# Kernel tuning notes

Measured on AMD Instinct MI355X. Metric: run time of the kernel, lower is better.

Reference implementation:

```python
import jax, jax.numpy as jnp
import numpy as np

N_FFT = 1024
N_STAGES = 3
N_SUB = N_FFT >> N_STAGES      # 128-point base IDFT
N_CHUNKS = 1 << N_STAGES       # 8 chunks after partial bit-reversal


def _mod_seq(order):
    mset = [0]
    for o in range(order):
        step = 2 ** o
        mset = [v for x in mset for v in (x, x + step)]
    return mset


def _perm_matrix(N, order):
    m = np.zeros((N, N), dtype=np.float32)
    base = 2 ** order
    k = 0
    for p in _mod_seq(order):
        for j in range(N // base):
            m[j * base + p, k] = 1.0
            k += 1
    return m


PERM = jnp.asarray(_perm_matrix(N_FFT, N_STAGES))
_idft = np.fft.ifft(np.eye(N_SUB))
IDFT_R = jnp.asarray(_idft.real.astype(np.float32))
IDFT_I = jnp.asarray(_idft.imag.astype(np.float32))


def _twiddle(n_fft_stage):
    w = np.exp(2j * np.pi / n_fft_stage) ** np.arange(n_fft_stage // 2)  # inverse sign
    return (jnp.asarray(w.real.astype(np.float32)),
            jnp.asarray(w.imag.astype(np.float32)))


TWIDDLES = []
_stage_size = N_FFT // 2 ** (N_STAGES - 1)
for _ in range(N_STAGES):
    TWIDDLES.append(_twiddle(_stage_size))
    _stage_size *= 2


def _idft_apply(re, im):
    yr = re @ IDFT_R.T - im @ IDFT_I.T
    yi = re @ IDFT_I.T + im @ IDFT_R.T
    return yr, yi


def _ifft_forward(re, im):
    # partial bit-reversal permutation then chunk
    re_p = jnp.split(re @ PERM, N_CHUNKS, axis=-1)
    im_p = jnp.split(im @ PERM, N_CHUNKS, axis=-1)
    ev_r, ev_i, od_r, od_i = [], [], [], []
    for j in range(N_CHUNKS // 2):
        er, ei = _idft_apply(re_p[2 * j], im_p[2 * j])
        o_r, o_i = _idft_apply(re_p[2 * j + 1], im_p[2 * j + 1])
        ev_r.append(er); ev_i.append(ei); od_r.append(o_r); od_i.append(o_i)
    # butterfly twiddle stages
    for tr, ti in TWIDDLES:
        ner, nei, nor, noi = [], [], [], []
        for i in range(len(ev_r)):
            todd_r = tr * od_r[i] - ti * od_i[i]
            todd_i = tr * od_i[i] + ti * od_r[i]
            real = jnp.concatenate([ev_r[i] + todd_r, ev_r[i] - todd_r], axis=-1)
            imag = jnp.concatenate([ev_i[i] + todd_i, ev_i[i] - todd_i], axis=-1)
            if i % 2 == 0:
                ner.append(real); nei.append(imag)
            else:
                nor.append(real); noi.append(imag)
        ev_r, ev_i, od_r, od_i = ner, nei, nor, noi
    scale = 1.0 / (1 << N_STAGES)  # IFFTNormalizer
    return ev_r[0] * scale, ev_i[0] * scale


def setup_inputs() -> dict:
    key = jax.random.key(0)
    k1, k2 = jax.random.split(key)
    re = jax.random.normal(k1, (8, 4096, N_FFT), dtype=jnp.float32)
    im = jax.random.normal(k2, (8, 4096, N_FFT), dtype=jnp.float32)
    return {"re": re, "im": im}


def reference(re, im):
    return _ifft_forward(re, im)
```

## Files before the change

### kernel.cpp

```cpp
#include <hip/hip_runtime.h>

#define NFFT 1024
#define NT   256
__device__ __forceinline__ int swz(int a) { return a + (a >> 5); }

template<int L, int M>
__device__ __forceinline__ void stage(const float* __restrict__ xr,
                                      const float* __restrict__ xi,
                                      float* __restrict__ yr,
                                      float* __restrict__ yi,
                                      int t) {
    const int k  = t & (M - 1);
    const int j  = t / M;
    const int rb = swz(t);

    float c0r = xr[rb];        float c0i = xi[rb];
    float c1r = xr[rb + 264];  float c1i = xi[rb + 264];
    float c2r = xr[rb + 528];  float c2i = xi[rb + 528];
    float c3r = xr[rb + 792];  float c3i = xi[rb + 792];

    float d0r = c0r + c2r, d0i = c0i + c2i;
    float d1r = c0r - c2r, d1i = c0i - c2i;
    float d2r = c1r + c3r, d2i = c1i + c3i;
    float d3r = c3i - c1i, d3i = c1r - c3r;

    float e0r = d0r + d2r, e0i = d0i + d2i;
    float e2r = d0r - d2r, e2i = d0i - d2i;
    float e1r = d1r + d3r, e1i = d1i + d3i;
    float e3r = d1r - d3r, e3i = d1i - d3i;

    float o1r, o1i, o2r, o2i, o3r, o3i;
    if (L == 1) {
        o1r = e1r; o1i = e1i; o2r = e2r; o2i = e2i; o3r = e3r; o3i = e3i;
    } else {
        const float base_ang = 6.28318530717958647692f / (float)(4 * L);
        float ang = base_ang * (float)j;
        float w1i, w1r;
        __sincosf(ang, &w1i, &w1r);
        float w2r = w1r * w1r - w1i * w1i;
        float w2i = 2.0f * w1r * w1i;
        float w3r = w2r * w1r - w2i * w1i;
        float w3i = w2r * w1i + w2i * w1r;
        o1r = w1r * e1r - w1i * e1i;  o1i = w1r * e1i + w1i * e1r;
        o2r = w2r * e2r - w2i * e2i;  o2i = w2r * e2i + w2i * e2r;
        o3r = w3r * e3r - w3i * e3i;  o3i = w3r * e3i + w3i * e3r;
    }

    const int wb = k + 4 * j * M;
    yr[swz(wb)]         = e0r;  yi[swz(wb)]         = e0i;
    yr[swz(wb + M)]     = o1r;  yi[swz(wb + M)]     = o1i;
    yr[swz(wb + 2 * M)] = o2r;  yi[swz(wb + 2 * M)] = o2i;
    yr[swz(wb + 3 * M)] = o3r;  yi[swz(wb + 3 * M)] = o3i;
}

__global__ __launch_bounds__(NT, 8) void ifft1024_kernel(
        const float* __restrict__ re, const float* __restrict__ im,
        float* __restrict__ out, size_t im_out_off) {
    __shared__ float Ar[1056], Ai[1056], Br[1056], Bi[1056];

    const int t = threadIdx.x;
    const size_t base = (size_t)blockIdx.x * NFFT;

    float4 r4 = *(const float4*)(re + base + 4 * t);
    float4 i4 = *(const float4*)(im + base + 4 * t);
    const int p = swz(4 * t);
    Ar[p] = r4.x; Ar[p + 1] = r4.y; Ar[p + 2] = r4.z; Ar[p + 3] = r4.w;
    Ai[p] = i4.x; Ai[p + 1] = i4.y; Ai[p + 2] = i4.z; Ai[p + 3] = i4.w;
    __syncthreads();

    stage<256, 1 >(Ar, Ai, Br, Bi, t); __syncthreads();
    stage<64,  4 >(Br, Bi, Ar, Ai, t); __syncthreads();
    stage<16,  16>(Ar, Ai, Br, Bi, t); __syncthreads();
    stage<4,   64>(Br, Bi, Ar, Ai, t); __syncthreads();
    stage<1,  256>(Ar, Ai, Br, Bi, t); __syncthreads();

    const float s = 1.0f / 1024.0f;
    float4 ro, io;
    ro.x = Br[p] * s; ro.y = Br[p + 1] * s; ro.z = Br[p + 2] * s; ro.w = Br[p + 3] * s;
    io.x = Bi[p] * s; io.y = Bi[p + 1] * s; io.z = Bi[p + 2] * s; io.w = Bi[p + 3] * s;

    *(float4*)(out + base + 4 * t)              = ro;
    *(float4*)(out + im_out_off + base + 4 * t) = io;
}

extern "C" void kernel_launch(void* const* d_in, const int* in_sizes, int n_in,
                              void* d_out, int out_size, void* d_ws, size_t ws_size,
                              hipStream_t stream) {
    const float* re = (const float*)d_in[0];
    const float* im = (const float*)d_in[1];
    float* out = (float*)d_out;
    const int rows = in_sizes[0] / NFFT;
    const size_t im_off = (size_t)in_sizes[0];

    hipLaunchKernelGGL(ifft1024_kernel, dim3(rows), dim3(NT), 0, stream,
                       re, im, out, im_off);
}
```

Baseline: 424.4 us.

## Fuse first and last radix-4 stages into global load and store

The first radix-4 stage now runs directly on strided global loads and the last stage writes directly to global memory. This removes two shared-memory round trips and two barriers. Global loads and stores become scalar, coalesced across threads, and use nontemporal hints. The L==1 special case is removed from the stage template, since the remaining uses all have L greater than 1.

```diff
diff --git a/kernel.cpp b/kernel.cpp
--- a/kernel.cpp
+++ b/kernel.cpp
@@ -29,22 +29,17 @@
     float e1r = d1r + d3r, e1i = d1i + d3i;
     float e3r = d1r - d3r, e3i = d1i - d3i;
 
-    float o1r, o1i, o2r, o2i, o3r, o3i;
-    if (L == 1) {
-        o1r = e1r; o1i = e1i; o2r = e2r; o2i = e2i; o3r = e3r; o3i = e3i;
-    } else {
-        const float base_ang = 6.28318530717958647692f / (float)(4 * L);
-        float ang = base_ang * (float)j;
-        float w1i, w1r;
-        __sincosf(ang, &w1i, &w1r);
-        float w2r = w1r * w1r - w1i * w1i;
-        float w2i = 2.0f * w1r * w1i;
-        float w3r = w2r * w1r - w2i * w1i;
-        float w3i = w2r * w1i + w2i * w1r;
-        o1r = w1r * e1r - w1i * e1i;  o1i = w1r * e1i + w1i * e1r;
-        o2r = w2r * e2r - w2i * e2i;  o2i = w2r * e2i + w2i * e2r;
-        o3r = w3r * e3r - w3i * e3i;  o3i = w3r * e3i + w3i * e3r;
-    }
+    const float base_ang = 6.28318530717958647692f / (float)(4 * L);
+    float ang = base_ang * (float)j;
+    float w1i, w1r;
+    __sincosf(ang, &w1i, &w1r);
+    float w2r = w1r * w1r - w1i * w1i;
+    float w2i = 2.0f * w1r * w1i;
+    float w3r = w2r * w1r - w2i * w1i;
+    float w3i = w2r * w1i + w2i * w1r;
+    float o1r = w1r * e1r - w1i * e1i;  float o1i = w1r * e1i + w1i * e1r;
+    float o2r = w2r * e2r - w2i * e2i;  float o2i = w2r * e2i + w2i * e2r;
+    float o3r = w3r * e3r - w3i * e3i;  float o3i = w3r * e3i + w3i * e3r;
 
     const int wb = k + 4 * j * M;
     yr[swz(wb)]         = e0r;  yi[swz(wb)]         = e0i;
@@ -61,26 +56,72 @@
     const int t = threadIdx.x;
     const size_t base = (size_t)blockIdx.x * NFFT;
 
-    float4 r4 = *(const float4*)(re + base + 4 * t);
-    float4 i4 = *(const float4*)(im + base + 4 * t);
-    const int p = swz(4 * t);
-    Ar[p] = r4.x; Ar[p + 1] = r4.y; Ar[p + 2] = r4.z; Ar[p + 3] = r4.w;
-    Ai[p] = i4.x; Ai[p + 1] = i4.y; Ai[p + 2] = i4.z; Ai[p + 3] = i4.w;
+    {
+        const float* rp = re + base + t;
+        const float* ip = im + base + t;
+        float c0r = __builtin_nontemporal_load(rp);
+        float c0i = __builtin_nontemporal_load(ip);
+        float c1r = __builtin_nontemporal_load(rp + 256);
+        float c1i = __builtin_nontemporal_load(ip + 256);
+        float c2r = __builtin_nontemporal_load(rp + 512);
+        float c2i = __builtin_nontemporal_load(ip + 512);
+        float c3r = __builtin_nontemporal_load(rp + 768);
+        float c3i = __builtin_nontemporal_load(ip + 768);
+
+        float d0r = c0r + c2r, d0i = c0i + c2i;
+        float d1r = c0r - c2r, d1i = c0i - c2i;
+        float d2r = c1r + c3r, d2i = c1i + c3i;
+        float d3r = c3i - c1i, d3i = c1r - c3r;
+
+        float e0r = d0r + d2r, e0i = d0i + d2i;
+        float e2r = d0r - d2r, e2i = d0i - d2i;
+        float e1r = d1r + d3r, e1i = d1i + d3i;
+        float e3r = d1r - d3r, e3i = d1i - d3i;
+
+        float ang = 6.28318530717958647692f / 1024.0f * (float)t;
+        float w1i, w1r;
+        __sincosf(ang, &w1i, &w1r);
+        float w2r = w1r * w1r - w1i * w1i;
+        float w2i = 2.0f * w1r * w1i;
+        float w3r = w2r * w1r - w2i * w1i;
+        float w3i = w2r * w1i + w2i * w1r;
+
+        const int wb = swz(4 * t);
+        Ar[wb]     = e0r;                   Ai[wb]     = e0i;
+        Ar[wb + 1] = w1r * e1r - w1i * e1i; Ai[wb + 1] = w1r * e1i + w1i * e1r;
+        Ar[wb + 2] = w2r * e2r - w2i * e2i; Ai[wb + 2] = w2r * e2i + w2i * e2r;
+        Ar[wb + 3] = w3r * e3r - w3i * e3i; Ai[wb + 3] = w3r * e3i + w3i * e3r;
+    }
     __syncthreads();
 
-    stage<256, 1 >(Ar, Ai, Br, Bi, t); __syncthreads();
-    stage<64,  4 >(Br, Bi, Ar, Ai, t); __syncthreads();
-    stage<16,  16>(Ar, Ai, Br, Bi, t); __syncthreads();
-    stage<4,   64>(Br, Bi, Ar, Ai, t); __syncthreads();
-    stage<1,  256>(Ar, Ai, Br, Bi, t); __syncthreads();
+    stage<64, 4 >(Ar, Ai, Br, Bi, t); __syncthreads();
+    stage<16, 16>(Br, Bi, Ar, Ai, t); __syncthreads();
+    stage<4,  64>(Ar, Ai, Br, Bi, t); __syncthreads();
 
-    const float s = 1.0f / 1024.0f;
-    float4 ro, io;
-    ro.x = Br[p] * s; ro.y = Br[p + 1] * s; ro.z = Br[p + 2] * s; ro.w = Br[p + 3] * s;
-    io.x = Bi[p] * s; io.y = Bi[p + 1] * s; io.z = Bi[p + 2] * s; io.w = Bi[p + 3] * s;
+    {
+        const int rb = swz(t);
+        float c0r = Br[rb];        float c0i = Bi[rb];
+        float c1r = Br[rb + 264];  float c1i = Bi[rb + 264];
+        float c2r = Br[rb + 528];  float c2i = Bi[rb + 528];
+        float c3r = Br[rb + 792];  float c3i = Bi[rb + 792];
 
-    *(float4*)(out + base + 4 * t)              = ro;
-    *(float4*)(out + im_out_off + base + 4 * t) = io;
+        float d0r = c0r + c2r, d0i = c0i + c2i;
+        float d1r = c0r - c2r, d1i = c0i - c2i;
+        float d2r = c1r + c3r, d2i = c1i + c3i;
+        float d3r = c3i - c1i, d3i = c1r - c3r;
+
+        const float s = 1.0f / 1024.0f;
+        float* orp = out + base + t;
+        float* oip = out + im_out_off + base + t;
+        __builtin_nontemporal_store((d0r + d2r) * s, orp);
+        __builtin_nontemporal_store((d0i + d2i) * s, oip);
+        __builtin_nontemporal_store((d1r + d3r) * s, orp + 256);
+        __builtin_nontemporal_store((d1i + d3i) * s, oip + 256);
+        __builtin_nontemporal_store((d0r - d2r) * s, orp + 512);
+        __builtin_nontemporal_store((d0i - d2i) * s, oip + 512);
+        __builtin_nontemporal_store((d1r - d3r) * s, orp + 768);
+        __builtin_nontemporal_store((d1i - d3i) * s, oip + 768);
+    }
 }
 
 extern "C" void kernel_launch(void* const* d_in, const int* in_sizes, int n_in,
```

Result: faster. 411.2 us (-3.1%).
